# Kernel tuning notes

Measured on AMD Instinct MI355X. Metric: run time of the kernel, lower is better.

## Reference

```python
import jax, jax.numpy as jnp
import numpy as np

N_TOPICS = 1024
TOPIC_DIM = 128
HIDDEN = 512
N_HEADS = 8
HEAD_DIM = HIDDEN // N_HEADS
N_LAYERS = 2
ALPHA = 0.2
TIME_DECAY = 0.1
BATCH = 8


def setup_inputs() -> dict:
    key = jax.random.key(0)
    ks = jax.random.split(key, 16)
    inp = {
        'topic_ids': jax.random.randint(ks[0], (BATCH,), 0, N_TOPICS, dtype=jnp.int32),
        'adj_matrix': jax.random.randint(ks[1], (BATCH, N_TOPICS, N_TOPICS), 0, 2, dtype=jnp.int32),
        'time_matrix': jax.random.uniform(ks[2], (BATCH, N_TOPICS, N_TOPICS), dtype=jnp.float32),
        'attractiveness': jax.random.normal(ks[3], (BATCH,), dtype=jnp.float32),
        # parameters (torch Linear convention: W [out,in], y = x@W.T + b)
        'topic_embedding': jax.random.normal(ks[4], (N_TOPICS, TOPIC_DIM), dtype=jnp.float32) * 0.1,
        'struct_W': jax.random.normal(ks[5], (HIDDEN, TOPIC_DIM), dtype=jnp.float32) * 0.05,
        'struct_b': jnp.zeros((HIDDEN,), dtype=jnp.float32),
        'attract_W': jax.random.normal(ks[6], (HIDDEN, 1), dtype=jnp.float32) * 0.05,
        'attract_b': jnp.zeros((HIDDEN,), dtype=jnp.float32),
        'gat_W': jax.random.normal(ks[7], (N_LAYERS, N_HEADS, HIDDEN, HEAD_DIM), dtype=jnp.float32) * 0.05,
        'gat_a': jax.random.normal(ks[8], (N_LAYERS, N_HEADS, 2 * HEAD_DIM, 1), dtype=jnp.float32) * 0.05,
        'fc1_W': jax.random.normal(ks[9], (HIDDEN, HIDDEN), dtype=jnp.float32) * 0.05,
        'fc1_b': jnp.zeros((HIDDEN,), dtype=jnp.float32),
        'fc2_W': jax.random.normal(ks[10], (1, HIDDEN), dtype=jnp.float32) * 0.05,
        'fc2_b': jnp.zeros((1,), dtype=jnp.float32),
    }
    return inp


def _gat_layer(node, adj, time_w, W, a):
    # node: [B,N,F], adj: [B,N,N] (0/1), time_w: [B,N,N]
    # W: [H,F,hd], a: [H,2*hd,1]
    h = jnp.einsum('bni,hio->bhno', node, W)  # [B,H,N,hd]
    # Additive attention: a = [a_src; a_dst] so e_ij = LeakyReLU(h_i.a_src + h_j.a_dst)
    a_src = a[:, :HEAD_DIM, 0]   # [H,hd]
    a_dst = a[:, HEAD_DIM:, 0]   # [H,hd]
    e_src = jnp.einsum('bhnd,hd->bhn', h, a_src)  # [B,H,N]
    e_dst = jnp.einsum('bhnd,hd->bhn', h, a_dst)  # [B,H,N]
    e = e_src[:, :, :, None] + e_dst[:, :, None, :]  # [B,H,N,N]
    e = jax.nn.leaky_relu(e, negative_slope=ALPHA)
    e = e * time_w[:, None, :, :]
    e = jnp.where(adj[:, None, :, :] == 0, -jnp.inf, e)
    attn = jax.nn.softmax(e, axis=-1)
    out = jnp.einsum('bhij,bhjd->bhid', attn, h)  # [B,H,N,hd]
    out = out.transpose(0, 2, 1, 3).reshape(node.shape[0], node.shape[1], -1)
    return jax.nn.elu(out)


def reference(topic_ids, adj_matrix, time_matrix, attractiveness,
              topic_embedding, struct_W, struct_b, attract_W, attract_b,
              gat_W, gat_a, fc1_W, fc1_b, fc2_W, fc2_b):
    # structural features for all topics -> hidden
    struct = topic_embedding @ struct_W.T + struct_b          # [N,hidden]
    attract = attractiveness[:, None] @ attract_W.T + attract_b  # [B,hidden]
    node = jnp.broadcast_to(struct[None], (BATCH, N_TOPICS, HIDDEN))
    # weighted co-occurrence time (eq.17)
    time_w = jnp.exp(-TIME_DECAY * (time_matrix.max() - time_matrix))  # [B,N,N]
    for l in range(N_LAYERS):
        node = _gat_layer(node, adj_matrix, time_w, gat_W[l], gat_a[l])
    # gather per-sample topic node feature
    topic_feat = jnp.take_along_axis(node, topic_ids[:, None, None].astype(jnp.int32), axis=1)[:, 0]  # [B,hidden]
    combined = topic_feat + attract
    hidden = jax.nn.relu(combined @ fc1_W.T + fc1_b)
    pred = hidden @ fc2_W.T + fc2_b  # [B,1]
    return pred
```

## Files before the change

### kernel.cpp

```cpp
#include <hip/hip_runtime.h>

#define NT 1024
#define TD 128
#define HID 512
#define NH 8
#define HD 64
#define NB 8

typedef unsigned short us;
typedef _Float16 h16;
typedef h16 half8 __attribute__((ext_vector_type(8)));
typedef h16 h16x2 __attribute__((ext_vector_type(2)));
typedef float f32x4 __attribute__((ext_vector_type(4)));

#define LOG2E 1.44269504f

extern "C" __device__ _Float16 __ocml_exp2_f16(_Float16);

__device__ __forceinline__ us f2h(float x) { return __builtin_bit_cast(us, (h16)x); }
__device__ __forceinline__ float h2f(us s) { return (float)__builtin_bit_cast(h16, s); }
__device__ __forceinline__ unsigned int pkh2(float a, float b) {
    auto v = __builtin_amdgcn_cvt_pkrtz(a, b);
    return __builtin_bit_cast(unsigned int, v);
}

__global__ __launch_bounds__(256) void kprep(const float* __restrict__ tm, float* __restrict__ part,
                                             const float* __restrict__ emb, const float* __restrict__ sW,
                                             const float* __restrict__ sb, us* __restrict__ node0b,
                                             const float* __restrict__ gW, us* __restrict__ Wt,
                                             const float* __restrict__ fc2b, float* __restrict__ out) {
    __shared__ __align__(16) float smf[8768];
    int bx = blockIdx.x, t = threadIdx.x;
    if (bx < 1024) {
        const float4* tm4 = (const float4*)tm;
        size_t base = (size_t)bx * 256 + t;
        float m = -1e30f;
        #pragma unroll
        for (int k = 0; k < 8; k++) {
            float4 v = tm4[base + (size_t)k * 262144];
            m = fmaxf(m, fmaxf(fmaxf(v.x, v.y), fmaxf(v.z, v.w)));
        }
        smf[t] = m; __syncthreads();
        for (int s = 128; s > 0; s >>= 1) { if (t < s) smf[t] = fmaxf(smf[t], smf[t + s]); __syncthreads(); }
        if (t == 0) part[bx] = smf[0];
    } else if (bx < 1152) {
        int g = bx - 1024; int iblk = g & 15, oseg = g >> 4;
        us* As = (us*)smf;
        us* Bs = (us*)smf + 64 * 136;
        const float4* esrc = (const float4*)(emb + (size_t)iblk * 64 * TD);
        const float4* wsrc = (const float4*)(sW + (size_t)oseg * 64 * TD);
        #pragma unroll
        for (int rep = 0; rep < 8; rep++) {
            int f = rep * 256 + t;
            int row = f >> 5, c4 = f & 31;
            float4 av = esrc[f];
            float4 bv = wsrc[f];
            uint2 pa, pb;
            pa.x = pkh2(av.x, av.y); pa.y = pkh2(av.z, av.w);
            pb.x = pkh2(bv.x, bv.y); pb.y = pkh2(bv.z, bv.w);
            *(uint2*)&As[row * 136 + c4 * 4] = pa;
            *(uint2*)&Bs[row * 136 + c4 * 4] = pb;
        }
        __syncthreads();
        int l = t & 63, w = t >> 6, m = l & 15, q = l >> 4;
        f32x4 acc[4];
        #pragma unroll
        for (int ot = 0; ot < 4; ot++) acc[ot] = (f32x4){0.f, 0.f, 0.f, 0.f};
        #pragma unroll
        for (int ks = 0; ks < 4; ks++) {
            half8 a = *(const half8*)&As[(w * 16 + m) * 136 + ks * 32 + q * 8];
            #pragma unroll
            for (int ot = 0; ot < 4; ot++) {
                half8 b = *(const half8*)&Bs[(ot * 16 + m) * 136 + ks * 32 + q * 8];
                acc[ot] = __builtin_amdgcn_mfma_f32_16x16x32_f16(a, b, acc[ot], 0, 0, 0);
            }
        }
        #pragma unroll
        for (int ot = 0; ot < 4; ot++) {
            int col = oseg * 64 + ot * 16 + m;
            float sbv = sb[col];
            #pragma unroll
            for (int rr = 0; rr < 4; rr++) {
                int rowi = iblk * 64 + w * 16 + q * 4 + rr;
                node0b[(size_t)rowi * HID + col] = f2h(acc[ot][rr] + sbv);
            }
        }
    } else {
        int g = bx - 1152; int lh = g >> 3, kt = g & 7;
        if (g == 0 && t < NB) out[t] = fc2b[0];
        float* tile = smf;
        const float4* src = (const float4*)(gW + ((size_t)lh * HID + kt * 64) * HD);
        #pragma unroll
        for (int rep = 0; rep < 4; rep++) {
            int f = rep * 256 + t;
            float4 v = src[f];
            int row = f >> 4, col = (f & 15) * 4;
            float* d = tile + row * 65 + col;
            d[0] = v.x; d[1] = v.y; d[2] = v.z; d[3] = v.w;
        }
        __syncthreads();
        int o = t >> 2, ks = (t & 3) * 16;
        us pk[16];
        #pragma unroll
        for (int j = 0; j < 16; j++) pk[j] = f2h(tile[(ks + j) * 65 + o]);
        us* dst = Wt + (size_t)lh * HD * HID + (size_t)o * HID + kt * 64 + ks;
        *(uint4*)dst = *(uint4*)pk;
        *(uint4*)(dst + 8) = *(uint4*)&pk[8];
    }
}

__device__ __forceinline__ void gemm_body(const us* __restrict__ A, const us* __restrict__ W,
                                          const float* __restrict__ gav,
                                          us* __restrict__ outT, us* __restrict__ outR,
                                          float* __restrict__ esO, float* __restrict__ edO,
                                          int iblk, int b, int h, int t, us* sm) {
    us* As = sm;
    us* Bs = sm + 2 * 4608;
    int row = t >> 2, ks = t & 3;
    int l = t & 63, w = t >> 6, m = l & 15, q = l >> 4;
    size_t arow0 = (size_t)(b * NT + iblk * 64);
    const us* ar = A + (arow0 + row) * HID + ks * 16;
    const us* br = W + ((size_t)(h * HD + row)) * HID + ks * 16;
    f32x4 acc[4];
    #pragma unroll
    for (int ot = 0; ot < 4; ot++) acc[ot] = (f32x4){0.f, 0.f, 0.f, 0.f};
    {
        uint4 x0 = *(const uint4*)ar, x1 = *(const uint4*)(ar + 8);
        uint4 y0 = *(const uint4*)br, y1 = *(const uint4*)(br + 8);
        *(uint4*)&As[row * 72 + ks * 16] = x0; *(uint4*)&As[row * 72 + ks * 16 + 8] = x1;
        *(uint4*)&Bs[row * 72 + ks * 16] = y0; *(uint4*)&Bs[row * 72 + ks * 16 + 8] = y1;
    }
    uint4 a0 = *(const uint4*)(ar + 64), a1 = *(const uint4*)(ar + 72);
    uint4 b0 = *(const uint4*)(br + 64), b1 = *(const uint4*)(br + 72);
    for (int it = 0; it < 8; it++) {
        int cur = it & 1, nxt = cur ^ 1;
        uint4 na0, na1, nb0, nb1;
        if (it < 6) {
            int k0 = (it + 2) * 64;
            na0 = *(const uint4*)(ar + k0); na1 = *(const uint4*)(ar + k0 + 8);
            nb0 = *(const uint4*)(br + k0); nb1 = *(const uint4*)(br + k0 + 8);
        }
        __syncthreads();
        if (it < 7) {
            *(uint4*)&As[nxt * 4608 + row * 72 + ks * 16] = a0;
            *(uint4*)&As[nxt * 4608 + row * 72 + ks * 16 + 8] = a1;
            *(uint4*)&Bs[nxt * 4608 + row * 72 + ks * 16] = b0;
            *(uint4*)&Bs[nxt * 4608 + row * 72 + ks * 16 + 8] = b1;
        }
        const us* Ac = As + cur * 4608; const us* Bc = Bs + cur * 4608;
        #pragma unroll
        for (int kt = 0; kt < 2; kt++) {
            half8 av = *(const half8*)&Ac[(w * 16 + m) * 72 + kt * 32 + q * 8];
            #pragma unroll
            for (int ot = 0; ot < 4; ot++) {
                half8 bv = *(const half8*)&Bc[(ot * 16 + m) * 72 + kt * 32 + q * 8];
                acc[ot] = __builtin_amdgcn_mfma_f32_16x16x32_f16(av, bv, acc[ot], 0, 0, 0);
            }
        }
        if (it < 6) { a0 = na0; a1 = na1; b0 = nb0; b1 = nb1; }
    }
    const float* gas = gav + h * 2 * HD;
    float gs[4], gd[4];
    #pragma unroll
    for (int ot = 0; ot < 4; ot++) { gs[ot] = gas[ot * 16 + m]; gd[ot] = gas[HD + ot * 16 + m]; }
    size_t ebase = ((size_t)b * NH + h) * NT + iblk * 64;
    #pragma unroll
    for (int rr = 0; rr < 4; rr++) {
        float s = 0.f, d = 0.f;
        #pragma unroll
        for (int ot = 0; ot < 4; ot++) { float v = acc[ot][rr]; s = fmaf(v, gs[ot], s); d = fmaf(v, gd[ot], d); }
        #pragma unroll
        for (int mask = 1; mask < 16; mask <<= 1) { s += __shfl_xor(s, mask); d += __shfl_xor(d, mask); }
        if (m == 0) {
            int rowi = w * 16 + q * 4 + rr;
            esO[ebase + rowi] = s;
            edO[ebase + rowi] = d;
        }
    }
    #pragma unroll
    for (int ot = 0; ot < 4; ot++) {
        int col = h * HD + ot * 16 + m;
        #pragma unroll
        for (int rr = 0; rr < 4; rr++) {
            int i_loc = w * 16 + q * 4 + rr;
            float v = acc[ot][rr];
            if (outT) outT[(size_t)col * NT + iblk * 64 + i_loc] = f2h(v);
            if (outR) outR[(arow0 + i_loc) * HID + col] = f2h(v);
        }
    }
}

__global__ __launch_bounds__(256) void kphase1(const float* __restrict__ tm, const int* __restrict__ adj,
                                               const float* __restrict__ part, us* __restrict__ TWb,
                                               const us* __restrict__ node0b, const us* __restrict__ Wt,
                                               const float* __restrict__ ga, us* __restrict__ Ht1,
                                               float* __restrict__ es1, float* __restrict__ ed1) {
    __shared__ __align__(16) us sm[4 * 4608];
    int bx = blockIdx.x, t = threadIdx.x;
    if (bx < 2048) {
        float* red = (float*)sm;
        float m = fmaxf(fmaxf(part[t * 4], part[t * 4 + 1]), fmaxf(part[t * 4 + 2], part[t * 4 + 3]));
        red[t] = m; __syncthreads();
        for (int s = 128; s > 0; s >>= 1) { if (t < s) red[t] = fmaxf(red[t], red[t + s]); __syncthreads(); }
        float tmx = red[0];
        const float C = 0.1f * LOG2E;
        const float NANF = __uint_as_float(0x7FC00000u);
        #pragma unroll
        for (int it = 0; it < 4; it++) {
            size_t idx = (((size_t)bx * 4 + it) * 256 + t) * 4;
            float4 tv = *(const float4*)(tm + idx);
            int4 av = *(const int4*)(adj + idx);
            float w0 = exp2f((tv.x - tmx) * C) * LOG2E;
            float w1 = exp2f((tv.y - tmx) * C) * LOG2E;
            float w2 = exp2f((tv.z - tmx) * C) * LOG2E;
            float w3 = exp2f((tv.w - tmx) * C) * LOG2E;
            w0 = av.x ? w0 : NANF;
            w1 = av.y ? w1 : NANF;
            w2 = av.z ? w2 : NANF;
            w3 = av.w ? w3 : NANF;
            uint2 pk;
            pk.x = pkh2(w0, w1);
            pk.y = pkh2(w2, w3);
            *(uint2*)&TWb[idx] = pk;
        }
    } else {
        int g = bx - 2048;
        gemm_body(node0b, Wt, ga, Ht1, nullptr, es1, ed1, g & 15, 0, g >> 4, t, sm);
    }
}

__global__ __launch_bounds__(256) void kgemm2(const us* __restrict__ node1b, const us* __restrict__ Wt2,
                                              const float* __restrict__ ga2, us* __restrict__ H2b,
                                              float* __restrict__ es2, float* __restrict__ ed2) {
    __shared__ __align__(16) us sm[4 * 4608];
    int n = blockIdx.x;
    int b = n & 7, k = n >> 3, iblk = k & 15, h = k >> 4;
    gemm_body(node1b, Wt2, ga2, nullptr, H2b, es2, ed2, iblk, b, h, threadIdx.x, sm);
}

__device__ __forceinline__ unsigned int p_word_fly(unsigned int tw, unsigned int ed, h16x2 es) {
    h16x2 t = __builtin_bit_cast(h16x2, tw);
    h16x2 d = __builtin_bit_cast(h16x2, ed);
    h16x2 e = es + d;
    h16x2 lk = e * (h16)0.2f;
    h16x2 el = __builtin_elementwise_max(e, lk);
    h16x2 mm = t * el;
    h16x2 p;
    p.x = __ocml_exp2_f16(mm.x);
    p.y = __ocml_exp2_f16(mm.y);
    h16x2 z = {(h16)0.0f, (h16)0.0f};
    h16x2 r = __builtin_elementwise_max(p, z);
    return __builtin_bit_cast(unsigned int, r);
}

__device__ __forceinline__ half8 p_frag(uint4 T, uint4 D, h16x2 es) {
    uint4 r;
    r.x = p_word_fly(T.x, D.x, es);
    r.y = p_word_fly(T.y, D.y, es);
    r.z = p_word_fly(T.z, D.z, es);
    r.w = p_word_fly(T.w, D.w, es);
    return __builtin_bit_cast(half8, r);
}

__global__ __launch_bounds__(256) void kattn1(const us* __restrict__ TWb, const us* __restrict__ Ht,
                                              const float* __restrict__ es1, const float* __restrict__ ed1,
                                              us* __restrict__ node1b) {
    int n = blockIdx.x;
    int b = n & 7, k = n >> 3;
    int i2 = k & 7, h = k >> 3;
    int t = threadIdx.x;
    __shared__ __align__(16) us Hs[2][64 * 72];
    __shared__ __align__(16) us edl[NT];
    __shared__ float invl_s[128];
    int l = t & 63, w = t >> 6, m = l & 15, q = l >> 4;
    {
        float4 ev = *(const float4*)&ed1[h * NT + t * 4];
        uint2 pk; pk.x = pkh2(ev.x, ev.y); pk.y = pkh2(ev.z, ev.w);
        *(uint2*)&edl[t * 4] = pk;
    }
    int rowA = i2 * 128 + w * 32 + m;
    h16 eA = (h16)es1[h * NT + rowA];
    h16 eB = (h16)es1[h * NT + rowA + 16];
    h16x2 esvA = {eA, eA}, esvB = {eB, eB};
    const us* twA = TWb + ((size_t)(b * NT) + rowA) * NT + q * 8;
    const us* twB = twA + (size_t)16 * NT;
    int hr = t >> 2, js = t & 3;
    const us* htrow = Ht + ((size_t)(h * HD) + hr) * NT + js * 16;
    f32x4 acc[2][4];
    #pragma unroll
    for (int ti = 0; ti < 2; ti++)
        #pragma unroll
        for (int ot = 0; ot < 4; ot++) acc[ti][ot] = (f32x4){0.f, 0.f, 0.f, 0.f};
    f32x4 acc1[2] = {(f32x4){0.f, 0.f, 0.f, 0.f}, (f32x4){0.f, 0.f, 0.f, 0.f}};
    h16 ov = (m == 0) ? (h16)1.0f : (h16)0.0f;
    half8 bones = {ov, ov, ov, ov, ov, ov, ov, ov};
    uint4 H0 = *(const uint4*)htrow, H1 = *(const uint4*)(htrow + 8);
    *(uint4*)&Hs[0][hr * 72 + js * 16] = H0;
    *(uint4*)&Hs[0][hr * 72 + js * 16 + 8] = H1;
    H0 = *(const uint4*)(htrow + 64); H1 = *(const uint4*)(htrow + 72);
    uint4 TA0 = *(const uint4*)twA,        TA1 = *(const uint4*)(twA + 32);
    uint4 TB0 = *(const uint4*)twB,        TB1 = *(const uint4*)(twB + 32);
    __syncthreads();
    for (int it = 0; it < 16; it++) {
        int cur = it & 1, nxt = cur ^ 1;
        int j0 = it * 64;
        uint4 nH0, nH1, nA0, nA1, nB0, nB1;
        if (it < 14) {
            nH0 = *(const uint4*)(htrow + j0 + 128);
            nH1 = *(const uint4*)(htrow + j0 + 136);
        }
        if (it < 15) {
            nA0 = *(const uint4*)(twA + j0 + 64);  nA1 = *(const uint4*)(twA + j0 + 96);
            nB0 = *(const uint4*)(twB + j0 + 64);  nB1 = *(const uint4*)(twB + j0 + 96);
        }
        uint4 D0 = *(const uint4*)&edl[j0 + q * 8];
        uint4 D1 = *(const uint4*)&edl[j0 + 32 + q * 8];
        half8 pA0 = p_frag(TA0, D0, esvA);
        half8 pA1 = p_frag(TA1, D1, esvA);
        half8 pB0 = p_frag(TB0, D0, esvB);
        half8 pB1 = p_frag(TB1, D1, esvB);
        __syncthreads();
        if (it < 15) {
            *(uint4*)&Hs[nxt][hr * 72 + js * 16] = H0;
            *(uint4*)&Hs[nxt][hr * 72 + js * 16 + 8] = H1;
        }
        const us* Hc = Hs[cur];
        #pragma unroll
        for (int ot = 0; ot < 4; ot++) {
            half8 bv0 = *(const half8*)&Hc[(ot * 16 + m) * 72 + q * 8];
            half8 bv1 = *(const half8*)&Hc[(ot * 16 + m) * 72 + 32 + q * 8];
            acc[0][ot] = __builtin_amdgcn_mfma_f32_16x16x32_f16(pA0, bv0, acc[0][ot], 0, 0, 0);
            acc[0][ot] = __builtin_amdgcn_mfma_f32_16x16x32_f16(pA1, bv1, acc[0][ot], 0, 0, 0);
            acc[1][ot] = __builtin_amdgcn_mfma_f32_16x16x32_f16(pB0, bv0, acc[1][ot], 0, 0, 0);
            acc[1][ot] = __builtin_amdgcn_mfma_f32_16x16x32_f16(pB1, bv1, acc[1][ot], 0, 0, 0);
        }
        acc1[0] = __builtin_amdgcn_mfma_f32_16x16x32_f16(pA0, bones, acc1[0], 0, 0, 0);
        acc1[0] = __builtin_amdgcn_mfma_f32_16x16x32_f16(pA1, bones, acc1[0], 0, 0, 0);
        acc1[1] = __builtin_amdgcn_mfma_f32_16x16x32_f16(pB0, bones, acc1[1], 0, 0, 0);
        acc1[1] = __builtin_amdgcn_mfma_f32_16x16x32_f16(pB1, bones, acc1[1], 0, 0, 0);
        if (it < 14) { H0 = nH0; H1 = nH1; }
        if (it < 15) { TA0 = nA0; TA1 = nA1; TB0 = nB0; TB1 = nB1; }
    }
    if (m == 0) {
        #pragma unroll
        for (int rr = 0; rr < 4; rr++) {
            invl_s[w * 32 + q * 4 + rr]      = 1.f / acc1[0][rr];
            invl_s[w * 32 + 16 + q * 4 + rr] = 1.f / acc1[1][rr];
        }
    }
    __syncthreads();
    size_t rbase = (size_t)(b * NT + i2 * 128);
    #pragma unroll
    for (int ti = 0; ti < 2; ti++) {
        #pragma unroll
        for (int ot = 0; ot < 4; ot++) {
            int col = h * HD + ot * 16 + m;
            #pragma unroll
            for (int rr = 0; rr < 4; rr++) {
                int rloc = w * 32 + ti * 16 + q * 4 + rr;
                float v = acc[ti][ot][rr] * invl_s[rloc];
                v = v > 0.f ? v : (__expf(v) - 1.f);
                node1b[(rbase + rloc) * HID + col] = f2h(v);
            }
        }
    }
}

__global__ __launch_bounds__(256) void kattn2a(const us* __restrict__ TWb, const us* __restrict__ H2b,
                                               const float* __restrict__ es2, const float* __restrict__ ed2,
                                               const int* __restrict__ topic_ids,
                                               float* __restrict__ ppv, float* __restrict__ pl) {
    int js = blockIdx.x, h = blockIdx.y, b = blockIdx.z;
    int t = threadIdx.x;
    __shared__ float pls[64];
    __shared__ float red[256];
    int qi = topic_ids[b];
    if (t < 64) {
        int j = js * 64 + t;
        float esq = es2[((size_t)b * NH + h) * NT + qi];
        float tw = h2f(TWb[((size_t)(b * NT) + qi) * NT + j]);
        float e = esq + ed2[((size_t)b * NH + h) * NT + j];
        e = fmaxf(e, 0.2f * e) * tw;
        float p = fmaxf(exp2f(e), 0.f);
        pls[t] = p;
        float lsum = p;
        #pragma unroll
        for (int mask = 1; mask < 64; mask <<= 1) lsum += __shfl_xor(lsum, mask);
        if (t == 0) pl[((size_t)b * NH + h) * 16 + js] = lsum;
    }
    __syncthreads();
    int o = t & 63, jg = t >> 6;
    float acc = 0.f;
    const us* hb = H2b + ((size_t)(b * NT) + js * 64 + jg * 16) * HID + h * HD + o;
    #pragma unroll
    for (int jj = 0; jj < 16; jj++)
        acc = fmaf(pls[jg * 16 + jj], h2f(hb[(size_t)jj * HID]), acc);
    red[t] = acc; __syncthreads();
    if (t < 64) {
        float pv = red[t] + red[t + 64] + red[t + 128] + red[t + 192];
        ppv[(((size_t)b * NH + h) * 16 + js) * HD + t] = pv;
    }
}

__global__ __launch_bounds__(256) void khead2(const float* __restrict__ ppv, const float* __restrict__ pl,
                                              const float* __restrict__ attr,
                                              const float* __restrict__ aW, const float* __restrict__ ab,
                                              const float* __restrict__ fc1W, const float* __restrict__ fc1b,
                                              const float* __restrict__ fc2W, float* __restrict__ out) {
    int kseg = blockIdx.x, b = blockIdx.y;
    int t = threadIdx.x;
    __shared__ float comb[HID];
    __shared__ float linv[NH];
    __shared__ float r2[256];
    if (t < NH) {
        float lsum = 0.f;
        #pragma unroll
        for (int js = 0; js < 16; js++) lsum += pl[((size_t)b * NH + t) * 16 + js];
        linv[t] = 1.f / lsum;
    }
    __syncthreads();
    float av = attr[b];
    for (int k = t; k < HID; k += 256) {
        int h = k >> 6, o = k & 63;
        float pv = 0.f;
        #pragma unroll
        for (int js = 0; js < 16; js++) pv += ppv[(((size_t)b * NH + h) * 16 + js) * HD + o];
        float v = pv * linv[h];
        v = v > 0.f ? v : (__expf(v) - 1.f);
        comb[k] = v + av * aW[k] + ab[k];
    }
    __syncthreads();
    int kk = kseg * 16 + (t >> 4);
    int j = t & 15;
    const float* row = fc1W + (size_t)kk * HID;
    float acc = 0.f;
    #pragma unroll 8
    for (int mi = 0; mi < 32; mi++) {
        int idx = mi * 16 + j;
        acc = fmaf(comb[idx], row[idx], acc);
    }
    #pragma unroll
    for (int mask = 1; mask < 16; mask <<= 1) acc += __shfl_xor(acc, mask);
    float partv = 0.f;
    if (j == 0) {
        float hk = fmaxf(acc + fc1b[kk], 0.f);
        partv = hk * fc2W[kk];
    }
    r2[t] = partv; __syncthreads();
    for (int s = 128; s > 0; s >>= 1) { if (t < s) r2[t] += r2[t + s]; __syncthreads(); }
    if (t == 0) atomicAdd(&out[b], r2[0]);
}

extern "C" void kernel_launch(void* const* d_in, const int* in_sizes, int n_in,
                              void* d_out, int out_size, void* d_ws, size_t ws_size,
                              hipStream_t stream) {
    const int*   topic_ids = (const int*)d_in[0];
    const int*   adj       = (const int*)d_in[1];
    const float* tm        = (const float*)d_in[2];
    const float* attr      = (const float*)d_in[3];
    const float* emb       = (const float*)d_in[4];
    const float* sW        = (const float*)d_in[5];
    const float* sb        = (const float*)d_in[6];
    const float* aW        = (const float*)d_in[7];
    const float* ab        = (const float*)d_in[8];
    const float* gW        = (const float*)d_in[9];
    const float* ga        = (const float*)d_in[10];
    const float* fc1W      = (const float*)d_in[11];
    const float* fc1b      = (const float*)d_in[12];
    const float* fc2W      = (const float*)d_in[13];
    const float* fc2b      = (const float*)d_in[14];
    float* out = (float*)d_out;

    char* p = (char*)d_ws;
    us* TWb    = (us*)p; p += sizeof(us) * (size_t)NB * NT * NT;
    us* node0b = (us*)p; p += sizeof(us) * (size_t)NT * HID;
    us* Wt     = (us*)p; p += sizeof(us) * (size_t)2 * NH * HD * HID;
    us* Ht1    = (us*)p; p += sizeof(us) * (size_t)HID * NT;
    us* node1b = (us*)p; p += sizeof(us) * (size_t)NB * NT * HID;
    us* H2b    = (us*)p; p += sizeof(us) * (size_t)NB * NT * HID;
    float* es1  = (float*)p; p += sizeof(float) * NH * NT;
    float* ed1  = (float*)p; p += sizeof(float) * NH * NT;
    float* es2  = (float*)p; p += sizeof(float) * NB * NH * NT;
    float* ed2  = (float*)p; p += sizeof(float) * NB * NH * NT;
    float* ppv  = (float*)p; p += sizeof(float) * NB * NH * 16 * HD;
    float* pl   = (float*)p; p += sizeof(float) * NB * NH * 16;
    float* part = (float*)p; p += sizeof(float) * 1024;

    kprep<<<1280, 256, 0, stream>>>(tm, part, emb, sW, sb, node0b, gW, Wt, fc2b, out);
    kphase1<<<2176, 256, 0, stream>>>(tm, adj, part, TWb, node0b, Wt, ga, Ht1, es1, ed1);
    kattn1<<<512, 256, 0, stream>>>(TWb, Ht1, es1, ed1, node1b);
    kgemm2<<<1024, 256, 0, stream>>>(node1b, Wt + (size_t)NH * HD * HID,
                                     ga + NH * 2 * HD, H2b, es2, ed2);
    kattn2a<<<dim3(16, NH, NB), 256, 0, stream>>>(TWb, H2b, es2, ed2, topic_ids, ppv, pl);
    khead2<<<dim3(32, NB), 256, 0, stream>>>(ppv, pl, attr, aW, ab, fc1W, fc1b, fc2W, out);
}
```

Before: 186.9 us.

## Compute time weights in the max-reduction pass and fold the max scale into attention scores

```diff
diff --git a/kernel.cpp b/kernel.cpp
--- a/kernel.cpp
+++ b/kernel.cpp
@@ -24,7 +24,8 @@
     return __builtin_bit_cast(unsigned int, v);
 }
 
-__global__ __launch_bounds__(256) void kprep(const float* __restrict__ tm, float* __restrict__ part,
+__global__ __launch_bounds__(256) void kprep(const float* __restrict__ tm, const int* __restrict__ adj,
+                                             float* __restrict__ part, us* __restrict__ TWb,
                                              const float* __restrict__ emb, const float* __restrict__ sW,
                                              const float* __restrict__ sb, us* __restrict__ node0b,
                                              const float* __restrict__ gW, us* __restrict__ Wt,
@@ -33,12 +34,29 @@
     int bx = blockIdx.x, t = threadIdx.x;
     if (bx < 1024) {
         const float4* tm4 = (const float4*)tm;
+        const int4* ad4 = (const int4*)adj;
         size_t base = (size_t)bx * 256 + t;
+        const float C = 0.1f * LOG2E;
+        const float NANF = __uint_as_float(0x7FC00000u);
         float m = -1e30f;
         #pragma unroll
         for (int k = 0; k < 8; k++) {
-            float4 v = tm4[base + (size_t)k * 262144];
+            size_t fi = base + (size_t)k * 262144;
+            float4 v = tm4[fi];
+            int4 av = ad4[fi];
             m = fmaxf(m, fmaxf(fmaxf(v.x, v.y), fmaxf(v.z, v.w)));
+            float w0 = exp2f(v.x * C) * LOG2E;
+            float w1 = exp2f(v.y * C) * LOG2E;
+            float w2 = exp2f(v.z * C) * LOG2E;
+            float w3 = exp2f(v.w * C) * LOG2E;
+            w0 = av.x ? w0 : NANF;
+            w1 = av.y ? w1 : NANF;
+            w2 = av.z ? w2 : NANF;
+            w3 = av.w ? w3 : NANF;
+            uint2 pk;
+            pk.x = pkh2(w0, w1);
+            pk.y = pkh2(w2, w3);
+            *(uint2*)&TWb[fi * 4] = pk;
         }
         smf[t] = m; __syncthreads();
         for (int s = 128; s > 0; s >>= 1) { if (t < s) smf[t] = fmaxf(smf[t], smf[t + s]); __syncthreads(); }
@@ -190,43 +208,12 @@
     }
 }
 
-__global__ __launch_bounds__(256) void kphase1(const float* __restrict__ tm, const int* __restrict__ adj,
-                                               const float* __restrict__ part, us* __restrict__ TWb,
-                                               const us* __restrict__ node0b, const us* __restrict__ Wt,
-                                               const float* __restrict__ ga, us* __restrict__ Ht1,
-                                               float* __restrict__ es1, float* __restrict__ ed1) {
+__global__ __launch_bounds__(256) void kgemm1(const us* __restrict__ node0b, const us* __restrict__ Wt,
+                                              const float* __restrict__ ga, us* __restrict__ Ht1,
+                                              float* __restrict__ es1, float* __restrict__ ed1) {
     __shared__ __align__(16) us sm[4 * 4608];
-    int bx = blockIdx.x, t = threadIdx.x;
-    if (bx < 2048) {
-        float* red = (float*)sm;
-        float m = fmaxf(fmaxf(part[t * 4], part[t * 4 + 1]), fmaxf(part[t * 4 + 2], part[t * 4 + 3]));
-        red[t] = m; __syncthreads();
-        for (int s = 128; s > 0; s >>= 1) { if (t < s) red[t] = fmaxf(red[t], red[t + s]); __syncthreads(); }
-        float tmx = red[0];
-        const float C = 0.1f * LOG2E;
-        const float NANF = __uint_as_float(0x7FC00000u);
-        #pragma unroll
-        for (int it = 0; it < 4; it++) {
-            size_t idx = (((size_t)bx * 4 + it) * 256 + t) * 4;
-            float4 tv = *(const float4*)(tm + idx);
-            int4 av = *(const int4*)(adj + idx);
-            float w0 = exp2f((tv.x - tmx) * C) * LOG2E;
-            float w1 = exp2f((tv.y - tmx) * C) * LOG2E;
-            float w2 = exp2f((tv.z - tmx) * C) * LOG2E;
-            float w3 = exp2f((tv.w - tmx) * C) * LOG2E;
-            w0 = av.x ? w0 : NANF;
-            w1 = av.y ? w1 : NANF;
-            w2 = av.z ? w2 : NANF;
-            w3 = av.w ? w3 : NANF;
-            uint2 pk;
-            pk.x = pkh2(w0, w1);
-            pk.y = pkh2(w2, w3);
-            *(uint2*)&TWb[idx] = pk;
-        }
-    } else {
-        int g = bx - 2048;
-        gemm_body(node0b, Wt, ga, Ht1, nullptr, es1, ed1, g & 15, 0, g >> 4, t, sm);
-    }
+    int g = blockIdx.x;
+    gemm_body(node0b, Wt, ga, Ht1, nullptr, es1, ed1, g & 15, 0, g >> 4, threadIdx.x, sm);
 }
 
 __global__ __launch_bounds__(256) void kgemm2(const us* __restrict__ node1b, const us* __restrict__ Wt2,
@@ -264,7 +251,7 @@
 
 __global__ __launch_bounds__(256) void kattn1(const us* __restrict__ TWb, const us* __restrict__ Ht,
                                               const float* __restrict__ es1, const float* __restrict__ ed1,
-                                              us* __restrict__ node1b) {
+                                              const float* __restrict__ part, us* __restrict__ node1b) {
     int n = blockIdx.x;
     int b = n & 7, k = n >> 3;
     int i2 = k & 7, h = k >> 3;
@@ -272,15 +259,22 @@
     __shared__ __align__(16) us Hs[2][64 * 72];
     __shared__ __align__(16) us edl[NT];
     __shared__ float invl_s[128];
+    __shared__ float reds[256];
     int l = t & 63, w = t >> 6, m = l & 15, q = l >> 4;
     {
+        float pm = fmaxf(fmaxf(part[t * 4], part[t * 4 + 1]), fmaxf(part[t * 4 + 2], part[t * 4 + 3]));
+        reds[t] = pm; __syncthreads();
+        for (int s = 128; s > 0; s >>= 1) { if (t < s) reds[t] = fmaxf(reds[t], reds[t + s]); __syncthreads(); }
+    }
+    float sfac = exp2f(-reds[0] * (0.1f * LOG2E));
+    {
         float4 ev = *(const float4*)&ed1[h * NT + t * 4];
-        uint2 pk; pk.x = pkh2(ev.x, ev.y); pk.y = pkh2(ev.z, ev.w);
+        uint2 pk; pk.x = pkh2(ev.x * sfac, ev.y * sfac); pk.y = pkh2(ev.z * sfac, ev.w * sfac);
         *(uint2*)&edl[t * 4] = pk;
     }
     int rowA = i2 * 128 + w * 32 + m;
-    h16 eA = (h16)es1[h * NT + rowA];
-    h16 eB = (h16)es1[h * NT + rowA + 16];
+    h16 eA = (h16)(es1[h * NT + rowA] * sfac);
+    h16 eB = (h16)(es1[h * NT + rowA + 16] * sfac);
     h16x2 esvA = {eA, eA}, esvB = {eB, eB};
     const us* twA = TWb + ((size_t)(b * NT) + rowA) * NT + q * 8;
     const us* twB = twA + (size_t)16 * NT;
@@ -368,19 +362,26 @@
 
 __global__ __launch_bounds__(256) void kattn2a(const us* __restrict__ TWb, const us* __restrict__ H2b,
                                                const float* __restrict__ es2, const float* __restrict__ ed2,
-                                               const int* __restrict__ topic_ids,
+                                               const int* __restrict__ topic_ids, const float* __restrict__ part,
                                                float* __restrict__ ppv, float* __restrict__ pl) {
     int js = blockIdx.x, h = blockIdx.y, b = blockIdx.z;
     int t = threadIdx.x;
     __shared__ float pls[64];
     __shared__ float red[256];
     int qi = topic_ids[b];
+    {
+        float pm = fmaxf(fmaxf(part[t * 4], part[t * 4 + 1]), fmaxf(part[t * 4 + 2], part[t * 4 + 3]));
+        red[t] = pm; __syncthreads();
+        for (int s = 128; s > 0; s >>= 1) { if (t < s) red[t] = fmaxf(red[t], red[t + s]); __syncthreads(); }
+    }
+    float sfac = exp2f(-red[0] * (0.1f * LOG2E));
+    __syncthreads();
     if (t < 64) {
         int j = js * 64 + t;
         float esq = es2[((size_t)b * NH + h) * NT + qi];
         float tw = h2f(TWb[((size_t)(b * NT) + qi) * NT + j]);
         float e = esq + ed2[((size_t)b * NH + h) * NT + j];
-        e = fmaxf(e, 0.2f * e) * tw;
+        e = fmaxf(e, 0.2f * e) * (tw * sfac);
         float p = fmaxf(exp2f(e), 0.f);
         pls[t] = p;
         float lsum = p;
@@ -486,11 +487,11 @@
     float* pl   = (float*)p; p += sizeof(float) * NB * NH * 16;
     float* part = (float*)p; p += sizeof(float) * 1024;
 
-    kprep<<<1280, 256, 0, stream>>>(tm, part, emb, sW, sb, node0b, gW, Wt, fc2b, out);
-    kphase1<<<2176, 256, 0, stream>>>(tm, adj, part, TWb, node0b, Wt, ga, Ht1, es1, ed1);
-    kattn1<<<512, 256, 0, stream>>>(TWb, Ht1, es1, ed1, node1b);
+    kprep<<<1280, 256, 0, stream>>>(tm, adj, part, TWb, emb, sW, sb, node0b, gW, Wt, fc2b, out);
+    kgemm1<<<128, 256, 0, stream>>>(node0b, Wt, ga, Ht1, es1, ed1);
+    kattn1<<<512, 256, 0, stream>>>(TWb, Ht1, es1, ed1, part, node1b);
     kgemm2<<<1024, 256, 0, stream>>>(node1b, Wt + (size_t)NH * HD * HID,
                                      ga + NH * 2 * HD, H2b, es2, ed2);
-    kattn2a<<<dim3(16, NH, NB), 256, 0, stream>>>(TWb, H2b, es2, ed2, topic_ids, ppv, pl);
+    kattn2a<<<dim3(16, NH, NB), 256, 0, stream>>>(TWb, H2b, es2, ed2, topic_ids, part, ppv, pl);
     khead2<<<dim3(32, NB), 256, 0, stream>>>(ppv, pl, attr, aW, ab, fc1W, fc1b, fc2W, out);
 }
```

Measured after the change: 179.3 us. 1.04x faster.
